# Kernel optimization log

Measured on AMD Instinct MI355X. Metric: run time of the kernel, lower is better.

## Reference

```python
import jax, jax.numpy as jnp
import numpy as np

DELTA_T = 0.05
LAMBDA = 1.0
LOG_2PI = float(np.log(2.0 * np.pi))


def _mlp(x, W1, b1, W2, b2):
    return jax.nn.relu(x @ W1 + b1) @ W2 + b2


def setup_inputs() -> dict:
    key = jax.random.key(0)
    ks = jax.random.split(key, 20)
    T, B, S = 128, 128, 8
    D_in, R, Z, H = 64, 256, 128, 512
    C, CH = 32, 64
    f = jax.random.normal
    inp = {
        "X": f(ks[0], (T, B, D_in), jnp.float32),
        "M": jax.random.uniform(ks[1], (T, B, D_in), jnp.float32),
        "cov": f(ks[2], (B, C), jnp.float32),
        "path_h": f(ks[3], (T, B, R), jnp.float32),
        "path_hpos": f(ks[4], (T, B, R), jnp.float32),
        "noise": f(ks[5], (T, B, S, Z), jnp.float32),
        # covariates_sde_map: C -> CH -> Z (tanh)
        "Wc1": f(ks[6], (C, CH), jnp.float32) / np.sqrt(C),
        "bc1": jnp.zeros((CH,), jnp.float32),
        "Wc2": f(ks[7], (CH, Z), jnp.float32) / np.sqrt(CH),
        "bc2": jnp.zeros((Z,), jnp.float32),
        # drift_model: R+Z -> H -> Z (tanh)
        "Wd1": f(ks[8], (R + Z, H), jnp.float32) / np.sqrt(R + Z),
        "bd1": jnp.zeros((H,), jnp.float32),
        "Wd2": f(ks[9], (H, Z), jnp.float32) / np.sqrt(H),
        "bd2": jnp.zeros((Z,), jnp.float32),
        # diffusion_model: R -> H -> Z
        "Wf1": f(ks[10], (R, H), jnp.float32) / np.sqrt(R),
        "bf1": jnp.zeros((H,), jnp.float32),
        "Wf2": f(ks[11], (H, Z), jnp.float32) / np.sqrt(H),
        "bf2": jnp.zeros((Z,), jnp.float32),
        # p_model: R+Z -> H -> 2*D_in (mean, logvar)
        "Wp1": f(ks[12], (R + Z, H), jnp.float32) / np.sqrt(R + Z),
        "bp1": jnp.zeros((H,), jnp.float32),
        "Wp2": f(ks[13], (H, 2 * D_in), jnp.float32) / np.sqrt(H),
        "bp2": jnp.zeros((2 * D_in,), jnp.float32),
    }
    return inp


def reference(X, M, cov, path_h, path_hpos, noise,
              Wc1, bc1, Wc2, bc2, Wd1, bd1, Wd2, bd2,
              Wf1, bf1, Wf2, bf2, Wp1, bp1, Wp2, bp2):
    T, B, _ = X.shape
    S = noise.shape[2]
    dt = jnp.float32(DELTA_T)
    sqrt_dt = jnp.sqrt(dt)

    # z0: [B, S, Z]
    z0 = jnp.tanh(_mlp(cov, Wc1, bc1, Wc2, bc2))[:, None, :]
    z0 = jnp.broadcast_to(z0, (B, S, z0.shape[-1]))

    def step(carry, xs):
        z, kld, recon = carry
        Xt, Mt_full, h_t, hpos_t, eps_t = xs
        hb = jnp.broadcast_to(h_t[:, None, :], (B, S, h_t.shape[-1]))       # [B,S,R]
        hposb = jnp.broadcast_to((h_t + hpos_t)[:, None, :], (B, S, h_t.shape[-1]))

        prior = 0.1 * jnp.tanh(_mlp(jnp.concatenate([hb, z], -1), Wd1, bd1, Wd2, bd2))
        poster = 0.1 * jnp.tanh(_mlp(jnp.concatenate([hposb, z], -1), Wd1, bd1, Wd2, bd2))
        diffusion = jnp.exp(_mlp(hb, Wf1, bf1, Wf2, bf2))                   # [B,S,Z]

        # Euler-Maruyama update (train=True: posterior drift)
        z = z + dt * poster + sqrt_dt * diffusion * eps_t

        p = _mlp(jnp.concatenate([hb, z], -1), Wp1, bp1, Wp2, bp2)          # [B,S,2*Din]
        mean, logvar = jnp.split(p, 2, axis=-1)

        Mt = jnp.mean(Mt_full, axis=-1, keepdims=True)                      # [B,1]
        errors = (prior - poster) / diffusion
        kld = kld + 0.5 * dt * jnp.sum(jnp.mean(errors ** 2, axis=1)) / B

        nll = 0.5 * (LOG_2PI + logvar + (Xt[:, None, :] - mean) ** 2 * jnp.exp(-logvar))
        recon_t = jnp.mean(nll, axis=1) * Mt                                # [B,Din]
        recon = recon + jnp.mean(jnp.sum(recon_t, axis=-1))
        return (z, kld, recon), None

    (z, loss_kld, loss_recon), _ = jax.lax.scan(
        step, (z0, jnp.float32(0.0), jnp.float32(0.0)),
        (X, M, path_h, path_hpos, noise))
    loss_total = loss_recon + LAMBDA * loss_kld
    return z, loss_total, loss_recon, loss_kld
```

## Files before the change

### kernel.cpp

```cpp
#include <hip/hip_runtime.h>
#include <hip/hip_bf16.h>
#include <math.h>

#define T_DIM 128
#define B_DIM 128
#define S_DIM 8
#define DIN   64
#define R_DIM 256
#define Z_DIM 128
#define H_DIM 512
#define C_DIM 32
#define CH_DIM 64

#define DT_F      0.05f
#define SQRT_DT_F 0.22360679774997896f
#define LOG_2PI_F 1.8378770664093453f

typedef _Float16 f16;
typedef __fp16 fp16x2 __attribute__((ext_vector_type(2)));
typedef _Float16 f16x8 __attribute__((ext_vector_type(8)));
typedef float f32x4 __attribute__((ext_vector_type(4)));
typedef unsigned u32x4 __attribute__((ext_vector_type(4)));

union U16x8 { uint4 u; f16x8 h; };

__device__ __forceinline__ f32x4 mfma16(const uint4& a, const uint4& b, f32x4 c) {
    U16x8 ua, ub; ua.u = a; ub.u = b;
    return __builtin_amdgcn_mfma_f32_16x16x32_f16(ua.h, ub.h, c, 0, 0, 0);
}

__device__ __forceinline__ f32x4 mfma16v(u32x4 a, u32x4 b, f32x4 c) {
    return __builtin_amdgcn_mfma_f32_16x16x32_f16(
        __builtin_bit_cast(f16x8, a), __builtin_bit_cast(f16x8, b), c, 0, 0, 0);
}

#define KEEPV(x) asm volatile("" : "+v"(x))

__device__ __forceinline__ unsigned pk2(float a, float b) {
    fp16x2 h = __builtin_amdgcn_cvt_pkrtz(a, b);
    return __builtin_bit_cast(unsigned, h);
}
__device__ __forceinline__ float upk_lo(unsigned u) {
    return (float)__builtin_bit_cast(f16, (unsigned short)(u & 0xffffu));
}
__device__ __forceinline__ float upk_hi(unsigned u) {
    return (float)__builtin_bit_cast(f16, (unsigned short)(u >> 16));
}

__device__ __forceinline__ float rcp_fast(float x) {
    return __builtin_amdgcn_rcpf(x);
}

__device__ __forceinline__ float tanh_fast(float x) {
    float ax = fabsf(x);
    float e  = __expf(-2.0f * ax);
    float r  = (1.0f - e) * rcp_fast(1.0f + e);
    return copysignf(r, x);
}

__global__ __launch_bounds__(256) void kw_frag(
    const float* __restrict__ Wd1, const float* __restrict__ Wd2,
    const float* __restrict__ Wp1, const float* __restrict__ Wp2,
    const float* __restrict__ Wf1, const float* __restrict__ Wf2,
    f16* __restrict__ WA, f16* __restrict__ WB,
    f16* __restrict__ WC, f16* __restrict__ WD,
    f16* __restrict__ W1A, f16* __restrict__ WF1,
    f16* __restrict__ WP1A, f16* __restrict__ WF2)
{
    int gid = blockIdx.x * 256 + threadIdx.x;
    const float* W; f16* dst; int k0, nktl, ld, off;
    if      (gid < 65536)  { W = Wd1; dst = WA;   k0 = 256; nktl = 2; ld = 512; off = gid; }
    else if (gid < 131072) { W = Wd2; dst = WB;   k0 = 0;   nktl = 4; ld = 128; off = gid - 65536; }
    else if (gid < 196608) { W = Wp1; dst = WC;   k0 = 256; nktl = 2; ld = 512; off = gid - 131072; }
    else if (gid < 262144) { W = Wp2; dst = WD;   k0 = 0;   nktl = 4; ld = 128; off = gid - 196608; }
    else if (gid < 393216) { W = Wd1; dst = W1A;  k0 = 0;   nktl = 3; ld = 512; off = gid - 262144; }
    else if (gid < 524288) { W = Wf1; dst = WF1;  k0 = 0;   nktl = 3; ld = 512; off = gid - 393216; }
    else if (gid < 655360) { W = Wp1; dst = WP1A; k0 = 0;   nktl = 3; ld = 512; off = gid - 524288; }
    else                   { W = Wf2; dst = WF2;  k0 = 0;   nktl = 4; ld = 128; off = gid - 655360; }
    int j = off & 7, l = (off >> 3) & 63, tile = off >> 9;
    int mt = tile >> nktl, kt = tile & ((1 << nktl) - 1);
    int lr = l & 15, lg = l >> 4;
    int c = mt * 16 + lr;
    int k = k0 + kt * 32 + 8 * lg + j;
    dst[off] = (f16)W[(size_t)k * ld + c];
}

__global__ __launch_bounds__(128) void k0_init(
    const float* __restrict__ cov,
    const float* __restrict__ Wc1, const float* __restrict__ bc1,
    const float* __restrict__ Wc2, const float* __restrict__ bc2,
    float* __restrict__ z_state, float* __restrict__ loss_acc)
{
    int b = blockIdx.x;
    int tid = threadIdx.x;
    __shared__ float covs[C_DIM];
    __shared__ float hid[CH_DIM];
    if (tid < C_DIM) covs[tid] = cov[b * C_DIM + tid];
    __syncthreads();
    if (tid < CH_DIM) {
        float a = bc1[tid];
        #pragma unroll
        for (int c = 0; c < C_DIM; ++c) a = fmaf(covs[c], Wc1[c * CH_DIM + tid], a);
        hid[tid] = fmaxf(a, 0.0f);
    }
    __syncthreads();
    float a = bc2[tid];
    #pragma unroll 8
    for (int h = 0; h < CH_DIM; ++h) a = fmaf(hid[h], Wc2[h * Z_DIM + tid], a);
    float z0 = tanh_fast(a);
    #pragma unroll
    for (int s = 0; s < S_DIM; ++s)
        z_state[((size_t)b * S_DIM + s) * Z_DIM + tid] = z0;
    if (b == 0 && tid < 2) loss_acc[tid] = 0.0f;
}

__global__ __launch_bounds__(512, 1) void k1_pre(
    const float* __restrict__ path_h, const float* __restrict__ path_hpos,
    const float* __restrict__ M,
    const f16* __restrict__ W1A, const f16* __restrict__ WF1,
    const f16* __restrict__ WP1A, const f16* __restrict__ WF2,
    const float* __restrict__ bd1, const float* __restrict__ bf1,
    const float* __restrict__ bf2, const float* __restrict__ bp1,
    f16* __restrict__ HprF, f16* __restrict__ HpoF, f16* __restrict__ HpF,
    float* __restrict__ Diff, float* __restrict__ MtM)
{
    const int base = blockIdx.x * 64;
    const int tid = threadIdx.x;
    const int wv = tid >> 6, l = tid & 63;
    const int lr = l & 15, lg = l >> 4;

    __shared__ uint4 ABf[2][4][8][64];
    __shared__ uint4 FHf[4][16][64];

    {
        int row = base + (tid >> 3), sg = tid & 7;
        const float4* mp = (const float4*)(M + (size_t)row * DIN + sg * 8);
        float4 m0 = mp[0], m1 = mp[1];
        float sm = m0.x + m0.y + m0.z + m0.w + m1.x + m1.y + m1.z + m1.w;
        sm += __shfl_xor(sm, 1);
        sm += __shfl_xor(sm, 2);
        sm += __shfl_xor(sm, 4);
        if (sg == 0) MtM[row] = sm * (1.0f / 64.0f);
    }

    for (int it = 0; it < 4; ++it) {
        int s = it * 512 + tid;
        int ktkg = s & 31, n = (s >> 5) & 15, nt = s >> 9;
        int kt = ktkg >> 2, kg = ktkg & 3;
        int row = base + nt * 16 + n;
        const float4* ph4 = (const float4*)(path_h    + (size_t)row * R_DIM + kt * 32 + kg * 8);
        const float4* pp4 = (const float4*)(path_hpos + (size_t)row * R_DIM + kt * 32 + kg * 8);
        float4 a0 = ph4[0], a1 = ph4[1];
        float4 p0 = pp4[0], p1 = pp4[1];
        uint4 ua, us;
        ua.x = pk2(a0.x, a0.y); ua.y = pk2(a0.z, a0.w);
        ua.z = pk2(a1.x, a1.y); ua.w = pk2(a1.z, a1.w);
        us.x = pk2(a0.x + p0.x, a0.y + p0.y); us.y = pk2(a0.z + p0.z, a0.w + p0.w);
        us.z = pk2(a1.x + p1.x, a1.y + p1.y); us.w = pk2(a1.z + p1.z, a1.w + p1.w);
        int ll = n + 16 * kg;
        ABf[0][nt][kt][ll] = ua;
        ABf[1][nt][kt][ll] = us;
    }
    __syncthreads();

    {
        f32x4 accP[4][4], accQ[4][4];
        #pragma unroll
        for (int mt = 0; mt < 4; ++mt)
            #pragma unroll
            for (int nt = 0; nt < 4; ++nt) { accP[mt][nt] = (f32x4)0.f; accQ[mt][nt] = (f32x4)0.f; }
        for (int kt = 0; kt < 8; ++kt) {
            uint4 wa[4], bA[4], bS[4];
            #pragma unroll
            for (int mt = 0; mt < 4; ++mt)
                wa[mt] = ((const uint4*)W1A)[(size_t)((wv * 4 + mt) * 8 + kt) * 64 + l];
            #pragma unroll
            for (int nt = 0; nt < 4; ++nt) { bA[nt] = ABf[0][nt][kt][l]; bS[nt] = ABf[1][nt][kt][l]; }
            #pragma unroll
            for (int mt = 0; mt < 4; ++mt)
                #pragma unroll
                for (int nt = 0; nt < 4; ++nt) {
                    accP[mt][nt] = mfma16(wa[mt], bA[nt], accP[mt][nt]);
                    accQ[mt][nt] = mfma16(wa[mt], bS[nt], accQ[mt][nt]);
                }
        }
        #pragma unroll
        for (int mt = 0; mt < 4; ++mt) {
            int c0 = wv * 64 + mt * 16 + 4 * lg;
            float4 bv = *(const float4*)&bd1[c0];
            #pragma unroll
            for (int nt = 0; nt < 4; ++nt) {
                size_t o = (size_t)(base + nt * 16 + lr) * H_DIM + c0;
                uint2 wp, wq;
                wp.x = pk2(accP[mt][nt][0] + bv.x, accP[mt][nt][1] + bv.y);
                wp.y = pk2(accP[mt][nt][2] + bv.z, accP[mt][nt][3] + bv.w);
                wq.x = pk2(accQ[mt][nt][0] + bv.x, accQ[mt][nt][1] + bv.y);
                wq.y = pk2(accQ[mt][nt][2] + bv.z, accQ[mt][nt][3] + bv.w);
                *(uint2*)&HprF[o] = wp;
                *(uint2*)&HpoF[o] = wq;
            }
        }
    }

    {
        f32x4 accH[4][4];
        #pragma unroll
        for (int mt = 0; mt < 4; ++mt)
            #pragma unroll
            for (int nt = 0; nt < 4; ++nt) accH[mt][nt] = (f32x4)0.f;
        for (int kt = 0; kt < 8; ++kt) {
            uint4 wa[4], bA[4];
            #pragma unroll
            for (int mt = 0; mt < 4; ++mt)
                wa[mt] = ((const uint4*)WP1A)[(size_t)((wv * 4 + mt) * 8 + kt) * 64 + l];
            #pragma unroll
            for (int nt = 0; nt < 4; ++nt) bA[nt] = ABf[0][nt][kt][l];
            #pragma unroll
            for (int mt = 0; mt < 4; ++mt)
                #pragma unroll
                for (int nt = 0; nt < 4; ++nt) accH[mt][nt] = mfma16(wa[mt], bA[nt], accH[mt][nt]);
        }
        #pragma unroll
        for (int mt = 0; mt < 4; ++mt) {
            int c0 = wv * 64 + mt * 16 + 4 * lg;
            float4 bv = *(const float4*)&bp1[c0];
            #pragma unroll
            for (int nt = 0; nt < 4; ++nt) {
                size_t o = (size_t)(base + nt * 16 + lr) * H_DIM + c0;
                uint2 wp;
                wp.x = pk2(accH[mt][nt][0] + bv.x, accH[mt][nt][1] + bv.y);
                wp.y = pk2(accH[mt][nt][2] + bv.z, accH[mt][nt][3] + bv.w);
                *(uint2*)&HpF[o] = wp;
            }
        }
    }

    {
        f32x4 accF[4][4];
        #pragma unroll
        for (int mt = 0; mt < 4; ++mt)
            #pragma unroll
            for (int nt = 0; nt < 4; ++nt) accF[mt][nt] = (f32x4)0.f;
        for (int kt = 0; kt < 8; ++kt) {
            uint4 wa[4], bA[4];
            #pragma unroll
            for (int mt = 0; mt < 4; ++mt)
                wa[mt] = ((const uint4*)WF1)[(size_t)((wv * 4 + mt) * 8 + kt) * 64 + l];
            #pragma unroll
            for (int nt = 0; nt < 4; ++nt) bA[nt] = ABf[0][nt][kt][l];
            #pragma unroll
            for (int mt = 0; mt < 4; ++mt)
                #pragma unroll
                for (int nt = 0; nt < 4; ++nt) accF[mt][nt] = mfma16(wa[mt], bA[nt], accF[mt][nt]);
        }
        #pragma unroll
        for (int mt = 0; mt < 4; ++mt) {
            int c0 = wv * 64 + mt * 16 + 4 * lg;
            float4 bv = *(const float4*)&bf1[c0];
            int kt2 = c0 >> 5;
            int l2  = lr + 16 * ((c0 >> 3) & 3);
            int half = (c0 & 7) >> 2;
            #pragma unroll
            for (int nt = 0; nt < 4; ++nt) {
                uint2 wp;
                wp.x = pk2(fmaxf(accF[mt][nt][0] + bv.x, 0.f), fmaxf(accF[mt][nt][1] + bv.y, 0.f));
                wp.y = pk2(fmaxf(accF[mt][nt][2] + bv.z, 0.f), fmaxf(accF[mt][nt][3] + bv.w, 0.f));
                ((uint2*)&FHf[nt][kt2][l2])[half] = wp;
            }
        }
    }
    __syncthreads();

    {
        f32x4 accD[4];
        #pragma unroll
        for (int nt = 0; nt < 4; ++nt) accD[nt] = (f32x4)0.f;
        for (int kt = 0; kt < 16; ++kt) {
            uint4 wf = ((const uint4*)WF2)[(size_t)(wv * 16 + kt) * 64 + l];
            #pragma unroll
            for (int nt = 0; nt < 4; ++nt) accD[nt] = mfma16(wf, FHf[nt][kt][l], accD[nt]);
        }
        int c0 = wv * 16 + 4 * lg;
        float4 bv = *(const float4*)&bf2[c0];
        #pragma unroll
        for (int nt = 0; nt < 4; ++nt) {
            float4 o;
            o.x = __expf(accD[nt][0] + bv.x);
            o.y = __expf(accD[nt][1] + bv.y);
            o.z = __expf(accD[nt][2] + bv.z);
            o.w = __expf(accD[nt][3] + bv.w);
            *(float4*)&Diff[(size_t)(base + nt * 16 + lr) * Z_DIM + c0] = o;
        }
    }
}

__global__ __launch_bounds__(512, 1) void k2_scan(
    const f16* __restrict__ WA, const f16* __restrict__ WB,
    const f16* __restrict__ HprF, const f16* __restrict__ HpoF,
    const float* __restrict__ Diff, const float* __restrict__ noise,
    const float* __restrict__ bd2,
    const float* __restrict__ z_state, unsigned* __restrict__ ztraj_u,
    float* __restrict__ out_z, float* __restrict__ loss_acc)
{
    const int b  = blockIdx.x >> 1;
    const int sh = blockIdx.x & 1;
    const int tid = threadIdx.x;
    const int wv = tid >> 6, l = tid & 63;
    const int lr = l & 15, lg = l >> 4;
    const bool owner = (lr < 4);
    const int lsafe = (l & 48) | (lr & 3);

    __shared__ u32x4 zfrag[4][64];
    __shared__ u32x4 phfrag[16][64];
    __shared__ u32x4 qhfrag[16][64];
    __shared__ float red2[512];

    u32x4 wa[4][4];
    #pragma unroll
    for (int mt = 0; mt < 4; ++mt)
        #pragma unroll
        for (int kt = 0; kt < 4; ++kt)
            wa[mt][kt] = ((const u32x4*)WA)[(size_t)((wv * 4 + mt) * 4 + kt) * 64 + l];
    u32x4 wb[16];
    #pragma unroll
    for (int kt = 0; kt < 16; ++kt)
        wb[kt] = ((const u32x4*)WB)[(size_t)(wv * 16 + kt) * 64 + l];
    #pragma unroll
    for (int mt = 0; mt < 4; ++mt)
        #pragma unroll
        for (int kt = 0; kt < 4; ++kt) KEEPV(wa[mt][kt]);
    #pragma unroll
    for (int kt = 0; kt < 16; ++kt) KEEPV(wb[kt]);

    const int j0 = wv * 16 + 4 * lg;
    const int srow = sh * 4 + lr;
    float zreg[4] = {0.f, 0.f, 0.f, 0.f};
    float bdv[4] = {0.f, 0.f, 0.f, 0.f};
    uint2* zslot = ((uint2*)&zfrag[wv >> 1][lr + 16 * (2 * (wv & 1) + (lg >> 1))]) + (lg & 1);
    if (owner) {
        *(float4*)zreg = *(const float4*)&z_state[((size_t)b * S_DIM + srow) * Z_DIM + j0];
        *(float4*)bdv  = *(const float4*)&bd2[j0];
        uint2 zz; zz.x = pk2(zreg[0], zreg[1]); zz.y = pk2(zreg[2], zreg[3]);
        *zslot = zz;
    }

    uint2 hp[4], hq[4];
    float4 dif, ep;
    if (owner) {
        #pragma unroll
        for (int mt = 0; mt < 4; ++mt) {
            int c0 = wv * 64 + mt * 16 + 4 * lg;
            hp[mt] = *(const uint2*)&HprF[(size_t)b * H_DIM + c0];
            hq[mt] = *(const uint2*)&HpoF[(size_t)b * H_DIM + c0];
        }
        dif = *(const float4*)&Diff[(size_t)b * Z_DIM + j0];
        ep  = *(const float4*)&noise[((size_t)b * S_DIM + srow) * Z_DIM + j0];
    }
    __syncthreads();

    float kacc = 0.f;

    for (int t = 0; t < T_DIM; ++t) {
        u32x4 zb[4];
        #pragma unroll
        for (int kt = 0; kt < 4; ++kt) zb[kt] = zfrag[kt][lsafe];
        #pragma unroll
        for (int mt = 0; mt < 4; ++mt) {
            f32x4 acc = (f32x4)0.f;
            #pragma unroll
            for (int kt = 0; kt < 4; ++kt) acc = mfma16v(wa[mt][kt], zb[kt], acc);
            if (owner) {
                fp16x2 zero2 = {(__fp16)0.f, (__fp16)0.f};
                fp16x2 a01 = __builtin_amdgcn_cvt_pkrtz(acc[0], acc[1]);
                fp16x2 a23 = __builtin_amdgcn_cvt_pkrtz(acc[2], acc[3]);
                fp16x2 p01 = __builtin_elementwise_max(a01 + __builtin_bit_cast(fp16x2, hp[mt].x), zero2);
                fp16x2 p23 = __builtin_elementwise_max(a23 + __builtin_bit_cast(fp16x2, hp[mt].y), zero2);
                fp16x2 q01 = __builtin_elementwise_max(a01 + __builtin_bit_cast(fp16x2, hq[mt].x), zero2);
                fp16x2 q23 = __builtin_elementwise_max(a23 + __builtin_bit_cast(fp16x2, hq[mt].y), zero2);
                int c0 = wv * 64 + mt * 16 + 4 * lg;
                int ktp = c0 >> 5;
                int l2  = lr + 16 * ((c0 >> 3) & 3);
                int half = (c0 & 7) >> 2;
                uint2 wp, wq;
                wp.x = __builtin_bit_cast(unsigned, p01); wp.y = __builtin_bit_cast(unsigned, p23);
                wq.x = __builtin_bit_cast(unsigned, q01); wq.y = __builtin_bit_cast(unsigned, q23);
                ((uint2*)&phfrag[ktp][l2])[half] = wp;
                ((uint2*)&qhfrag[ktp][l2])[half] = wq;
            }
        }

        int tn = (t + 1 < T_DIM) ? (t + 1) : t;
        uint2 hpn[4], hqn[4];
        float4 difn, epn;
        if (owner) {
            size_t hbn = ((size_t)tn * B_DIM + b) * H_DIM;
            #pragma unroll
            for (int mt = 0; mt < 4; ++mt) {
                int c0 = wv * 64 + mt * 16 + 4 * lg;
                hpn[mt] = *(const uint2*)&HprF[hbn + c0];
                hqn[mt] = *(const uint2*)&HpoF[hbn + c0];
            }
            difn = *(const float4*)&Diff[((size_t)tn * B_DIM + b) * Z_DIM + j0];
            epn  = *(const float4*)&noise[(((size_t)tn * B_DIM + b) * S_DIM + srow) * Z_DIM + j0];
        }
        __syncthreads();

        f32x4 aP = (f32x4)0.f, aQ = (f32x4)0.f;
        #pragma unroll
        for (int kt = 0; kt < 16; ++kt) {
            u32x4 pb = phfrag[kt][lsafe];
            u32x4 qb = qhfrag[kt][lsafe];
            aP = mfma16v(wb[kt], pb, aP);
            aQ = mfma16v(wb[kt], qb, aQ);
        }
        if (owner) {
            const float* difp = (const float*)&dif;
            const float* epp  = (const float*)&ep;
            #pragma unroll
            for (int i = 0; i < 4; ++i) {
                float pr = 0.1f * tanh_fast(aP[i] + bdv[i]);
                float po = 0.1f * tanh_fast(aQ[i] + bdv[i]);
                float dv = difp[i];
                zreg[i] = zreg[i] + DT_F * po + SQRT_DT_F * dv * epp[i];
                float e = (pr - po) * rcp_fast(dv);
                kacc = fmaf(e, e, kacc);
            }
            uint2 zz; zz.x = pk2(zreg[0], zreg[1]); zz.y = pk2(zreg[2], zreg[3]);
            *zslot = zz;
            *(uint2*)&ztraj_u[((size_t)t * 1024 + (size_t)b * S_DIM + srow) * 64 + (j0 >> 1)] = zz;
        }
        #pragma unroll
        for (int mt = 0; mt < 4; ++mt) { hp[mt] = hpn[mt]; hq[mt] = hqn[mt]; }
        dif = difn; ep = epn;
        __syncthreads();
    }

    if (owner)
        *(float4*)&out_z[((size_t)b * S_DIM + srow) * Z_DIM + j0] = *(const float4*)zreg;

    red2[tid] = kacc;
    __syncthreads();
    for (int st = 256; st > 0; st >>= 1) {
        if (tid < st) red2[tid] += red2[tid + st];
        __syncthreads();
    }
    if (tid == 0) atomicAdd(loss_acc + 0, red2[0]);
}

__global__ __launch_bounds__(512, 2) void k3_recon(
    const f16* __restrict__ WC, const f16* __restrict__ WD,
    const f16* __restrict__ HpF, const unsigned* __restrict__ ztraj_u,
    const float* __restrict__ X, const float* __restrict__ MtM,
    const float* __restrict__ bp2, float* __restrict__ loss_acc)
{
    const int t  = blockIdx.x >> 5;
    const int b0 = (blockIdx.x & 31) * 4;
    const int tid = threadIdx.x;
    const int wv = tid >> 6, l = tid & 63;
    const int lr = l & 15, lg = l >> 4;

    __shared__ uint4 zfrag[4][2][64];
    __shared__ uint4 pwfrag[16][2][64];
    __shared__ float obuf[128][33];
    __shared__ float red2[512];

    uint4 wc[4][4];
    #pragma unroll
    for (int mt = 0; mt < 4; ++mt)
        #pragma unroll
        for (int kt = 0; kt < 4; ++kt)
            wc[mt][kt] = ((const uint4*)WC)[(size_t)((wv * 4 + mt) * 4 + kt) * 64 + l];
    uint4 wd[16];
    #pragma unroll
    for (int kt = 0; kt < 16; ++kt)
        wd[kt] = ((const uint4*)WD)[(size_t)(wv * 16 + kt) * 64 + l];

    {
        int kt = tid >> 7;
        int nt = (tid >> 6) & 1;
        int ll = tid & 63;
        int n = ll & 15, kg = ll >> 4;
        int rl = nt * 16 + n;
        size_t grow = (size_t)t * 1024 + (size_t)b0 * S_DIM + rl;
        zfrag[kt][nt][ll] = *(const uint4*)&ztraj_u[grow * 64 + kt * 16 + kg * 4];
    }
    __syncthreads();

    f16* pwf = (f16*)pwfrag;
    #pragma unroll
    for (int nt = 0; nt < 2; ++nt) {
        #pragma unroll
        for (int mt = 0; mt < 4; ++mt) {
            f32x4 acc = (f32x4)0.f;
            #pragma unroll
            for (int kt = 0; kt < 4; ++kt) acc = mfma16(wc[mt][kt], zfrag[kt][nt][l], acc);
            int c0 = wv * 64 + mt * 16 + 4 * lg;
            int rl = nt * 16 + lr;
            int bb = b0 + (rl >> 3);
            size_t hbs = ((size_t)t * B_DIM + bb) * H_DIM;
            uint2 hpv = *(const uint2*)&HpF[hbs + c0];
            float p0 = fmaxf(acc[0] + upk_lo(hpv.x), 0.f);
            float p1 = fmaxf(acc[1] + upk_hi(hpv.x), 0.f);
            float p2 = fmaxf(acc[2] + upk_lo(hpv.y), 0.f);
            float p3 = fmaxf(acc[3] + upk_hi(hpv.y), 0.f);
            int ktp = c0 >> 5;
            int lp  = lr + 16 * ((c0 >> 3) & 3);
            int off = c0 & 7;
            uint2 wp; wp.x = pk2(p0, p1); wp.y = pk2(p2, p3);
            *(uint2*)&pwf[(size_t)((ktp * 2 + nt) * 64 + lp) * 8 + off] = wp;
        }
    }
    __syncthreads();

    #pragma unroll
    for (int nt = 0; nt < 2; ++nt) {
        f32x4 acc = (f32x4)0.f;
        #pragma unroll
        for (int kt = 0; kt < 16; ++kt) acc = mfma16(wd[kt], pwfrag[kt][nt][l], acc);
        int m0 = wv * 16 + 4 * lg;
        int row = nt * 16 + lr;
        #pragma unroll
        for (int i = 0; i < 4; ++i) obuf[m0 + i][row] = acc[i];
    }
    __syncthreads();

    float racc = 0.f;
    {
        int row = tid >> 4;
        int d4 = (tid & 15) * 4;
        int bb = b0 + (row >> 3);
        float mt = MtM[(size_t)t * B_DIM + bb];
        #pragma unroll
        for (int i = 0; i < 4; ++i) {
            int d = d4 + i;
            float mean = obuf[d][row] + bp2[d];
            float lv   = obuf[d + 64][row] + bp2[64 + d];
            float xv = X[((size_t)t * B_DIM + bb) * DIN + d];
            float dm = xv - mean;
            float nll = 0.5f * (LOG_2PI_F + lv + dm * dm * __expf(-lv));
            racc = fmaf(mt, nll, racc);
        }
    }
    red2[tid] = racc;
    __syncthreads();
    for (int st = 256; st > 0; st >>= 1) {
        if (tid < st) red2[tid] += red2[tid + st];
        __syncthreads();
    }
    if (tid == 0) atomicAdd(loss_acc + 1, red2[0]);
}

__global__ void k4_final(const float* __restrict__ loss_acc, float* __restrict__ out)
{
    if (threadIdx.x == 0 && blockIdx.x == 0) {
        float kld   = loss_acc[0] * (0.5f * DT_F / (float)(B_DIM * S_DIM));
        float recon = loss_acc[1] * (1.0f / (float)(B_DIM * S_DIM));
        out[131072] = recon + kld;
        out[131073] = recon;
        out[131074] = kld;
    }
}

extern "C" void kernel_launch(void* const* d_in, const int* in_sizes, int n_in,
                              void* d_out, int out_size, void* d_ws, size_t ws_size,
                              hipStream_t stream)
{
    const float* X        = (const float*)d_in[0];
    const float* M        = (const float*)d_in[1];
    const float* cov      = (const float*)d_in[2];
    const float* path_h   = (const float*)d_in[3];
    const float* path_hpos= (const float*)d_in[4];
    const float* noise    = (const float*)d_in[5];
    const float* Wc1 = (const float*)d_in[6];
    const float* bc1 = (const float*)d_in[7];
    const float* Wc2 = (const float*)d_in[8];
    const float* bc2 = (const float*)d_in[9];
    const float* Wd1 = (const float*)d_in[10];
    const float* bd1 = (const float*)d_in[11];
    const float* Wd2 = (const float*)d_in[12];
    const float* bd2 = (const float*)d_in[13];
    const float* Wf1 = (const float*)d_in[14];
    const float* bf1 = (const float*)d_in[15];
    const float* Wf2 = (const float*)d_in[16];
    const float* bf2 = (const float*)d_in[17];
    const float* Wp1 = (const float*)d_in[18];
    const float* bp1 = (const float*)d_in[19];
    const float* Wp2 = (const float*)d_in[20];
    const float* bp2 = (const float*)d_in[21];
    float* out = (float*)d_out;

    char* ws = (char*)d_ws;
    size_t o = 0;
    float* z_state = (float*)(ws + o); o += 524288;
    float* loss    = (float*)(ws + o); o += 256;
    f16* WA   = (f16*)(ws + o); o += 131072;
    f16* WB   = (f16*)(ws + o); o += 131072;
    f16* WC   = (f16*)(ws + o); o += 131072;
    f16* WD   = (f16*)(ws + o); o += 131072;
    f16* W1A  = (f16*)(ws + o); o += 262144;
    f16* WF1  = (f16*)(ws + o); o += 262144;
    f16* WP1A = (f16*)(ws + o); o += 262144;
    f16* WF2  = (f16*)(ws + o); o += 131072;
    f16* HprF = (f16*)(ws + o); o += 16777216;
    f16* HpoF = (f16*)(ws + o); o += 16777216;
    f16* HpF  = (f16*)(ws + o); o += 16777216;
    float* Diff = (float*)(ws + o); o += 8388608;
    float* MtM  = (float*)(ws + o); o += 65536;
    unsigned* ztraj = (unsigned*)(ws + o); o += 33554432;

    kw_frag<<<2816, 256, 0, stream>>>(Wd1, Wd2, Wp1, Wp2, Wf1, Wf2,
                                      WA, WB, WC, WD, W1A, WF1, WP1A, WF2);
    k0_init<<<B_DIM, 128, 0, stream>>>(cov, Wc1, bc1, Wc2, bc2, z_state, loss);
    k1_pre<<<256, 512, 0, stream>>>(path_h, path_hpos, M,
                                    W1A, WF1, WP1A, WF2,
                                    bd1, bf1, bf2, bp1,
                                    HprF, HpoF, HpF, Diff, MtM);
    k2_scan<<<256, 512, 0, stream>>>(WA, WB, HprF, HpoF, Diff, noise, bd2,
                                     z_state, ztraj, out, loss);
    k3_recon<<<4096, 512, 0, stream>>>(WC, WD, HpF, ztraj, X, MtM, bp2, loss);
    k4_final<<<1, 64, 0, stream>>>(loss, out);
}
```

Before: 591.3 us.

## Pack 16 sample rows per scan block to fill MFMA columns, pin weights in AGPRs

The sequential scan kernel previously used only 4 of the 16 MFMA B-columns per block, with 256 blocks each handling half a batch element. Each block now processes 16 rows (two batch elements of 8 samples), so every lane does useful work and the grid drops to 64 blocks. Weight fragments are now held in accumulator registers through a per-iteration asm constraint, freeing VGPRs for the extra live state. The cost is far fewer blocks on the GPU, so fewer CUs are busy during the latency-bound time loop, while the total MFMA work per block stays the same.

```diff
diff --git a/kernel.cpp b/kernel.cpp
--- a/kernel.cpp
+++ b/kernel.cpp
@@ -34,7 +34,7 @@
         __builtin_bit_cast(f16x8, a), __builtin_bit_cast(f16x8, b), c, 0, 0, 0);
 }
 
-#define KEEPV(x) asm volatile("" : "+v"(x))
+#define KEEPA(x) asm volatile("" : "+a"(x))
 
 __device__ __forceinline__ unsigned pk2(float a, float b) {
     fp16x2 h = __builtin_amdgcn_cvt_pkrtz(a, b);
@@ -302,13 +302,12 @@
     const float* __restrict__ z_state, unsigned* __restrict__ ztraj_u,
     float* __restrict__ out_z, float* __restrict__ loss_acc)
 {
-    const int b  = blockIdx.x >> 1;
-    const int sh = blockIdx.x & 1;
+    const int bk = blockIdx.x;
     const int tid = threadIdx.x;
     const int wv = tid >> 6, l = tid & 63;
     const int lr = l & 15, lg = l >> 4;
-    const bool owner = (lr < 4);
-    const int lsafe = (l & 48) | (lr & 3);
+    const int b   = bk * 2 + (lr >> 3);
+    const int row = bk * 16 + lr;
 
     __shared__ u32x4 zfrag[4][64];
     __shared__ u32x4 phfrag[16][64];
@@ -325,74 +324,72 @@
     #pragma unroll
     for (int kt = 0; kt < 16; ++kt)
         wb[kt] = ((const u32x4*)WB)[(size_t)(wv * 16 + kt) * 64 + l];
-    #pragma unroll
-    for (int mt = 0; mt < 4; ++mt)
-        #pragma unroll
-        for (int kt = 0; kt < 4; ++kt) KEEPV(wa[mt][kt]);
-    #pragma unroll
-    for (int kt = 0; kt < 16; ++kt) KEEPV(wb[kt]);
 
     const int j0 = wv * 16 + 4 * lg;
-    const int srow = sh * 4 + lr;
-    float zreg[4] = {0.f, 0.f, 0.f, 0.f};
-    float bdv[4] = {0.f, 0.f, 0.f, 0.f};
+    float zreg[4], bdv[4];
+    *(float4*)zreg = *(const float4*)&z_state[(size_t)row * Z_DIM + j0];
+    *(float4*)bdv  = *(const float4*)&bd2[j0];
     uint2* zslot = ((uint2*)&zfrag[wv >> 1][lr + 16 * (2 * (wv & 1) + (lg >> 1))]) + (lg & 1);
-    if (owner) {
-        *(float4*)zreg = *(const float4*)&z_state[((size_t)b * S_DIM + srow) * Z_DIM + j0];
-        *(float4*)bdv  = *(const float4*)&bd2[j0];
+    {
         uint2 zz; zz.x = pk2(zreg[0], zreg[1]); zz.y = pk2(zreg[2], zreg[3]);
         *zslot = zz;
     }
 
     uint2 hp[4], hq[4];
     float4 dif, ep;
-    if (owner) {
+    {
+        size_t hb0 = (size_t)b * H_DIM;
         #pragma unroll
         for (int mt = 0; mt < 4; ++mt) {
             int c0 = wv * 64 + mt * 16 + 4 * lg;
-            hp[mt] = *(const uint2*)&HprF[(size_t)b * H_DIM + c0];
-            hq[mt] = *(const uint2*)&HpoF[(size_t)b * H_DIM + c0];
+            hp[mt] = *(const uint2*)&HprF[hb0 + c0];
+            hq[mt] = *(const uint2*)&HpoF[hb0 + c0];
         }
         dif = *(const float4*)&Diff[(size_t)b * Z_DIM + j0];
-        ep  = *(const float4*)&noise[((size_t)b * S_DIM + srow) * Z_DIM + j0];
+        ep  = *(const float4*)&noise[(size_t)row * Z_DIM + j0];
     }
     __syncthreads();
 
     float kacc = 0.f;
 
     for (int t = 0; t < T_DIM; ++t) {
+        #pragma unroll
+        for (int mt = 0; mt < 4; ++mt)
+            #pragma unroll
+            for (int kt = 0; kt < 4; ++kt) KEEPA(wa[mt][kt]);
+        #pragma unroll
+        for (int kt = 0; kt < 16; ++kt) KEEPA(wb[kt]);
+
         u32x4 zb[4];
         #pragma unroll
-        for (int kt = 0; kt < 4; ++kt) zb[kt] = zfrag[kt][lsafe];
+        for (int kt = 0; kt < 4; ++kt) zb[kt] = zfrag[kt][l];
         #pragma unroll
         for (int mt = 0; mt < 4; ++mt) {
             f32x4 acc = (f32x4)0.f;
             #pragma unroll
             for (int kt = 0; kt < 4; ++kt) acc = mfma16v(wa[mt][kt], zb[kt], acc);
-            if (owner) {
-                fp16x2 zero2 = {(__fp16)0.f, (__fp16)0.f};
-                fp16x2 a01 = __builtin_amdgcn_cvt_pkrtz(acc[0], acc[1]);
-                fp16x2 a23 = __builtin_amdgcn_cvt_pkrtz(acc[2], acc[3]);
-                fp16x2 p01 = __builtin_elementwise_max(a01 + __builtin_bit_cast(fp16x2, hp[mt].x), zero2);
-                fp16x2 p23 = __builtin_elementwise_max(a23 + __builtin_bit_cast(fp16x2, hp[mt].y), zero2);
-                fp16x2 q01 = __builtin_elementwise_max(a01 + __builtin_bit_cast(fp16x2, hq[mt].x), zero2);
-                fp16x2 q23 = __builtin_elementwise_max(a23 + __builtin_bit_cast(fp16x2, hq[mt].y), zero2);
-                int c0 = wv * 64 + mt * 16 + 4 * lg;
-                int ktp = c0 >> 5;
-                int l2  = lr + 16 * ((c0 >> 3) & 3);
-                int half = (c0 & 7) >> 2;
-                uint2 wp, wq;
-                wp.x = __builtin_bit_cast(unsigned, p01); wp.y = __builtin_bit_cast(unsigned, p23);
-                wq.x = __builtin_bit_cast(unsigned, q01); wq.y = __builtin_bit_cast(unsigned, q23);
-                ((uint2*)&phfrag[ktp][l2])[half] = wp;
-                ((uint2*)&qhfrag[ktp][l2])[half] = wq;
-            }
+            fp16x2 zero2 = {(__fp16)0.f, (__fp16)0.f};
+            fp16x2 a01 = __builtin_amdgcn_cvt_pkrtz(acc[0], acc[1]);
+            fp16x2 a23 = __builtin_amdgcn_cvt_pkrtz(acc[2], acc[3]);
+            fp16x2 p01 = __builtin_elementwise_max(a01 + __builtin_bit_cast(fp16x2, hp[mt].x), zero2);
+            fp16x2 p23 = __builtin_elementwise_max(a23 + __builtin_bit_cast(fp16x2, hp[mt].y), zero2);
+            fp16x2 q01 = __builtin_elementwise_max(a01 + __builtin_bit_cast(fp16x2, hq[mt].x), zero2);
+            fp16x2 q23 = __builtin_elementwise_max(a23 + __builtin_bit_cast(fp16x2, hq[mt].y), zero2);
+            int c0 = wv * 64 + mt * 16 + 4 * lg;
+            int ktp = c0 >> 5;
+            int l2  = lr + 16 * ((c0 >> 3) & 3);
+            int half = (c0 & 7) >> 2;
+            uint2 wp, wq;
+            wp.x = __builtin_bit_cast(unsigned, p01); wp.y = __builtin_bit_cast(unsigned, p23);
+            wq.x = __builtin_bit_cast(unsigned, q01); wq.y = __builtin_bit_cast(unsigned, q23);
+            ((uint2*)&phfrag[ktp][l2])[half] = wp;
+            ((uint2*)&qhfrag[ktp][l2])[half] = wq;
         }
 
         int tn = (t + 1 < T_DIM) ? (t + 1) : t;
         uint2 hpn[4], hqn[4];
         float4 difn, epn;
-        if (owner) {
+        {
             size_t hbn = ((size_t)tn * B_DIM + b) * H_DIM;
             #pragma unroll
             for (int mt = 0; mt < 4; ++mt) {
@@ -401,19 +398,19 @@
                 hqn[mt] = *(const uint2*)&HpoF[hbn + c0];
             }
             difn = *(const float4*)&Diff[((size_t)tn * B_DIM + b) * Z_DIM + j0];
-            epn  = *(const float4*)&noise[(((size_t)tn * B_DIM + b) * S_DIM + srow) * Z_DIM + j0];
+            epn  = *(const float4*)&noise[((size_t)tn * 1024 + row) * Z_DIM + j0];
         }
         __syncthreads();
 
         f32x4 aP = (f32x4)0.f, aQ = (f32x4)0.f;
         #pragma unroll
         for (int kt = 0; kt < 16; ++kt) {
-            u32x4 pb = phfrag[kt][lsafe];
-            u32x4 qb = qhfrag[kt][lsafe];
+            u32x4 pb = phfrag[kt][l];
+            u32x4 qb = qhfrag[kt][l];
             aP = mfma16v(wb[kt], pb, aP);
             aQ = mfma16v(wb[kt], qb, aQ);
         }
-        if (owner) {
+        {
             const float* difp = (const float*)&dif;
             const float* epp  = (const float*)&ep;
             #pragma unroll
@@ -427,7 +424,7 @@
             }
             uint2 zz; zz.x = pk2(zreg[0], zreg[1]); zz.y = pk2(zreg[2], zreg[3]);
             *zslot = zz;
-            *(uint2*)&ztraj_u[((size_t)t * 1024 + (size_t)b * S_DIM + srow) * 64 + (j0 >> 1)] = zz;
+            *(uint2*)&ztraj_u[((size_t)t * 1024 + row) * 64 + (j0 >> 1)] = zz;
         }
         #pragma unroll
         for (int mt = 0; mt < 4; ++mt) { hp[mt] = hpn[mt]; hq[mt] = hqn[mt]; }
@@ -435,8 +432,7 @@
         __syncthreads();
     }
 
-    if (owner)
-        *(float4*)&out_z[((size_t)b * S_DIM + srow) * Z_DIM + j0] = *(const float4*)zreg;
+    *(float4*)&out_z[(size_t)row * Z_DIM + j0] = *(const float4*)zreg;
 
     red2[tid] = kacc;
     __syncthreads();
@@ -615,8 +611,8 @@
                                     W1A, WF1, WP1A, WF2,
                                     bd1, bf1, bf2, bp1,
                                     HprF, HpoF, HpF, Diff, MtM);
-    k2_scan<<<256, 512, 0, stream>>>(WA, WB, HprF, HpoF, Diff, noise, bd2,
-                                     z_state, ztraj, out, loss);
+    k2_scan<<<64, 512, 0, stream>>>(WA, WB, HprF, HpoF, Diff, noise, bd2,
+                                    z_state, ztraj, out, loss);
     k3_recon<<<4096, 512, 0, stream>>>(WC, WD, HpF, ztraj, X, MtM, bp2, loss);
     k4_final<<<1, 64, 0, stream>>>(loss, out);
 }
```

Result: faster. 555.7 us (-6.0%).
